# Performance work log

Measured on AMD Instinct MI355X. Metric: run time of the kernel, lower is better.

## Reference

```python
import jax, jax.numpy as jnp
import numpy as np

N = 20000      # num_nodes
B = 16         # batch
F = 64         # input_dim
K = 2          # max_diffusion_step
M = K + 1      # num_matrices
OUT = 64       # output_dim
E = 640000     # nnz of sparse support (avg degree 32)
BIAS_START = 1.414


def setup_inputs() -> dict:
    key = jax.random.key(0)
    ks = jax.random.split(key, 6)
    inputs = jax.random.normal(ks[0], (B, N, F), dtype=jnp.float32)
    sp_rows = jnp.sort(jax.random.randint(ks[1], (E,), 0, N, dtype=jnp.int32))
    sp_cols = jax.random.randint(ks[2], (E,), 0, N, dtype=jnp.int32)
    # scale values ~1/degree so the Chebyshev recursion stays numerically tame
    sp_vals = jax.random.uniform(ks[3], (E,), dtype=jnp.float32) / 32.0
    # xavier_normal_ with gain=1.414 on [F*M, OUT]
    std = 1.414 * (2.0 / (F * M + OUT)) ** 0.5
    weight = jax.random.normal(ks[4], (F * M, OUT), dtype=jnp.float32) * std
    biases = jnp.full((OUT,), BIAS_START, dtype=jnp.float32)
    return {"inputs": inputs, "sp_rows": sp_rows, "sp_cols": sp_cols,
            "sp_vals": sp_vals, "weight": weight, "biases": biases}


def _spmm(rows, cols, vals, x):
    # sparse [N,N] @ dense [N,C] via gather + segment_sum over edges
    return jax.ops.segment_sum(vals[:, None] * x[cols], rows, num_segments=N)


def reference(inputs, sp_rows, sp_cols, sp_vals, weight, biases):
    b, n, f = inputs.shape
    # [B,N,F] -> [N,F,B] -> [N, F*B]  (matches torch transpose/reshape order)
    x0 = jnp.transpose(inputs, (1, 2, 0)).reshape(n, f * b)
    xs = [x0]
    x1 = _spmm(sp_rows, sp_cols, sp_vals, x0)
    xs.append(x1)
    for _ in range(2, K + 1):
        x2 = 2.0 * _spmm(sp_rows, sp_cols, sp_vals, x1) - x0
        xs.append(x2)
        x1, x0 = x2, x1
    # [M, N, F, B] -> [B, N, F, M] -> [B*N, F*M]
    x = jnp.stack(xs, axis=0).reshape(M, n, f, b)
    x = jnp.transpose(x, (3, 1, 2, 0)).reshape(b * n, f * M)
    return x @ weight + biases
```

## Files before the change

### kernel.cpp

```cpp
#include <hip/hip_runtime.h>

#define NN 20000
#define EE 640000
#define CAP 2048
#define WTP 200

typedef __attribute__((ext_vector_type(8))) short short8;
typedef __attribute__((ext_vector_type(4))) float float4v;
typedef __attribute__((ext_vector_type(2))) float float2v;

__device__ __forceinline__ unsigned bf16rn(float x) {
    unsigned u = __float_as_uint(x);
    return (u + 0x7FFFu + ((u >> 16) & 1u)) >> 16;
}
__device__ __forceinline__ unsigned pack2(float a, float b) {
    return bf16rn(a) | (bf16rn(b) << 16);
}
__device__ __forceinline__ float bflo(unsigned u) { return __uint_as_float(u << 16); }
__device__ __forceinline__ float bfhi(unsigned u) { return __uint_as_float(u & 0xFFFF0000u); }

__global__ __launch_bounds__(256) void prep_k(
    const float* __restrict__ inp, unsigned* __restrict__ xb,
    const int* __restrict__ rows, int* __restrict__ rp,
    const float* __restrict__ W, unsigned short* __restrict__ wt,
    int nCast) {
    int bid = blockIdx.x, t = threadIdx.x;
    if (bid < nCast) {
        int i = bid * 256 + t;
        int n = i >> 7, c = i & 127;
        int b = c >> 3, f8 = c & 7;
        const float* p = inp + ((size_t)b * NN + n) * 64 + f8 * 8;
        float4 u0 = *(const float4*)(p);
        float4 u1 = *(const float4*)(p + 4);
        uint4 o;
        o.x = pack2(u0.x, u0.y); o.y = pack2(u0.z, u0.w);
        o.z = pack2(u1.x, u1.y); o.w = pack2(u1.z, u1.w);
        *(uint4*)(xb + (size_t)n * 512 + c * 4) = o;
    } else if (bid < nCast + 79) {
        int r = (bid - nCast) * 256 + t;
        if (r > NN) return;
        int lo = 0, hi = EE;
        while (lo < hi) {
            int mid = (lo + hi) >> 1;
            if (rows[mid] < r) lo = mid + 1; else hi = mid;
        }
        rp[r] = lo;
    } else {
        int i = (bid - nCast - 79) * 256 + t;
        if (i >= 64 * 192) return;
        int o = i / 192, kp = i - o * 192;
        int m = kp >> 6, f = kp & 63;
        float w = W[(f * 3 + m) * 64 + o];
        if (m == 0) w -= W[(f * 3 + 2) * 64 + o];
        else if (m == 2) w += w;
        wt[o * WTP + kp] = (unsigned short)bf16rn(w);
    }
}

__device__ __forceinline__ void accum(const uint4& q, int vbits,
                                      float2v& ac0, float2v& ac1,
                                      float2v& ac2, float2v& ac3) {
    float v_ = __int_as_float(vbits);
    float2v vv = {v_, v_};
    float2v p0 = {bflo(q.x), bfhi(q.x)};
    float2v p1 = {bflo(q.y), bfhi(q.y)};
    float2v p2 = {bflo(q.z), bfhi(q.z)};
    float2v p3 = {bflo(q.w), bfhi(q.w)};
    ac0 = __builtin_elementwise_fma(vv, p0, ac0);
    ac1 = __builtin_elementwise_fma(vv, p1, ac1);
    ac2 = __builtin_elementwise_fma(vv, p2, ac2);
    ac3 = __builtin_elementwise_fma(vv, p3, ac3);
}

__global__ __launch_bounds__(256, 8) void spmm_bf16_k(
    const unsigned* __restrict__ src, const int* __restrict__ cols,
    const float* __restrict__ vals, const int* __restrict__ rp,
    unsigned* __restrict__ dst) {
    __shared__ int2 lcv[CAP];
    int bid = blockIdx.x;
    int xcd = bid & 7, j = bid >> 3;
    int chunk = j % 625;
    int s = xcd + ((j / 625) << 3);
    int t = threadIdx.x;
    int n0 = chunk * 32;
    int eBase = rp[n0];
    int eCap = min(rp[n0 + 32], eBase + CAP);
    for (int i = eBase + t; i < eCap; i += 256)
        lcv[i - eBase] = make_int2(cols[i], __float_as_int(vals[i]));
    __syncthreads();

    int node = n0 + (t >> 3);
    unsigned tOff = (unsigned)(s * 128 + (t & 7) * 16);
    const char* sb = (const char*)src;
    int e0 = rp[node], e1 = rp[node + 1];
    int eL = min(e1, eCap);
    int le = e0 - eBase, lEnd = eL - eBase;
    float2v ac0 = {0,0}, ac1 = {0,0}, ac2 = {0,0}, ac3 = {0,0};

    int e = le;
    for (; e + 4 <= lEnd; e += 4) {
        int2 c0 = lcv[e],     c1 = lcv[e + 1];
        int2 c2 = lcv[e + 2], c3 = lcv[e + 3];
        uint4 q0 = *(const uint4*)(sb + (((unsigned)c0.x << 11) + tOff));
        uint4 q1 = *(const uint4*)(sb + (((unsigned)c1.x << 11) + tOff));
        uint4 q2 = *(const uint4*)(sb + (((unsigned)c2.x << 11) + tOff));
        uint4 q3 = *(const uint4*)(sb + (((unsigned)c3.x << 11) + tOff));
        accum(q0, c0.y, ac0, ac1, ac2, ac3);
        accum(q1, c1.y, ac0, ac1, ac2, ac3);
        accum(q2, c2.y, ac0, ac1, ac2, ac3);
        accum(q3, c3.y, ac0, ac1, ac2, ac3);
    }
    for (; e < lEnd; ++e) {
        int2 cv = lcv[e];
        uint4 q = *(const uint4*)(sb + (((unsigned)cv.x << 11) + tOff));
        accum(q, cv.y, ac0, ac1, ac2, ac3);
    }
    for (int a = lEnd + eBase; a < e1; ++a) {
        int c = cols[a];
        uint4 q = *(const uint4*)(sb + (((unsigned)c << 11) + tOff));
        accum(q, __float_as_int(vals[a]), ac0, ac1, ac2, ac3);
    }
    uint4 o;
    o.x = pack2(ac0[0], ac0[1]); o.y = pack2(ac1[0], ac1[1]);
    o.z = pack2(ac2[0], ac2[1]); o.w = pack2(ac3[0], ac3[1]);
    *(uint4*)((char*)dst + (size_t)node * 2048 + tOff) = o;
}

__global__ __launch_bounds__(256, 8) void spmm1_f32_k(
    const float* __restrict__ inputs, const int* __restrict__ cols,
    const float* __restrict__ vals, const int* __restrict__ rp,
    unsigned* __restrict__ y1) {
    __shared__ int2 lcv[CAP];
    int s = blockIdx.y, t = threadIdx.x;
    int n0 = blockIdx.x * 32;
    int eBase = rp[n0];
    int eCap = min(rp[n0 + 32], eBase + CAP);
    for (int i = eBase + t; i < eCap; i += 256)
        lcv[i - eBase] = make_int2(cols[i], __float_as_int(vals[i]));
    __syncthreads();

    int node = n0 + (t >> 3);
    const float* sp = inputs + (size_t)(s >> 1) * NN * 64 + (s & 1) * 32 + (t & 7) * 4;
    int e0 = rp[node], e1 = rp[node + 1];
    int eL = min(e1, eCap);
    float4 acc = make_float4(0.f, 0.f, 0.f, 0.f);
    #pragma unroll 2
    for (int e = e0; e < eL; ++e) {
        int2 cv = lcv[e - eBase];
        float v = __int_as_float(cv.y);
        float4 xv = *(const float4*)(sp + (size_t)cv.x * 64);
        acc.x += v * xv.x; acc.y += v * xv.y; acc.z += v * xv.z; acc.w += v * xv.w;
    }
    for (int e = eL; e < e1; ++e) {
        int c = cols[e]; float v = vals[e];
        float4 xv = *(const float4*)(sp + (size_t)c * 64);
        acc.x += v * xv.x; acc.y += v * xv.y; acc.z += v * xv.z; acc.w += v * xv.w;
    }
    uint2 o; o.x = pack2(acc.x, acc.y); o.y = pack2(acc.z, acc.w);
    *(uint2*)(y1 + (size_t)node * 512 + (s >> 1) * 32 + (s & 1) * 16 + (t & 7) * 2) = o;
}

__global__ __launch_bounds__(256) void gemm_k(
    const float* __restrict__ inputs, const unsigned* __restrict__ xb,
    const unsigned* __restrict__ y1, const unsigned* __restrict__ y2,
    const unsigned short* __restrict__ wt, const float* __restrict__ bias,
    float* __restrict__ out) {
    __shared__ unsigned short wl[64 * WTP];
    int t = threadIdx.x;
    for (int i = t; i < 1600; i += 256)
        ((uint4*)wl)[i] = ((const uint4*)wt)[i];
    __syncthreads();

    int w = t >> 6, l = t & 63;
    int lr = l & 15, lq = l >> 4;
    int n0 = blockIdx.x * 64 + w * 16;
    int nA = min(n0 + lr, NN - 1);
    float bv0 = bias[lr], bv1 = bias[16 + lr], bv2 = bias[32 + lr], bv3 = bias[48 + lr];

    #pragma unroll 2
    for (int bb = 0; bb < 4; ++bb) {
        int b = blockIdx.y * 4 + bb;
        const unsigned* p1 = y1 + (size_t)nA * 512 + b * 32 + lq * 4;
        const unsigned* p2 = y2 + (size_t)nA * 512 + b * 32 + lq * 4;

        short8 a[6];
        if (xb) {
            const unsigned* p0 = xb + (size_t)nA * 512 + b * 32 + lq * 4;
            a[0] = *(const short8*)(p0);
            a[1] = *(const short8*)(p0 + 16);
        } else {
            const float* px = inputs + ((size_t)b * NN + nA) * 64 + lq * 8;
            float4 u0 = *(const float4*)(px);
            float4 u1 = *(const float4*)(px + 4);
            float4 u2 = *(const float4*)(px + 32);
            float4 u3 = *(const float4*)(px + 36);
            short8 t0, t1;
            t0[0] = (short)bf16rn(u0.x); t0[1] = (short)bf16rn(u0.y);
            t0[2] = (short)bf16rn(u0.z); t0[3] = (short)bf16rn(u0.w);
            t0[4] = (short)bf16rn(u1.x); t0[5] = (short)bf16rn(u1.y);
            t0[6] = (short)bf16rn(u1.z); t0[7] = (short)bf16rn(u1.w);
            t1[0] = (short)bf16rn(u2.x); t1[1] = (short)bf16rn(u2.y);
            t1[2] = (short)bf16rn(u2.z); t1[3] = (short)bf16rn(u2.w);
            t1[4] = (short)bf16rn(u3.x); t1[5] = (short)bf16rn(u3.y);
            t1[6] = (short)bf16rn(u3.z); t1[7] = (short)bf16rn(u3.w);
            a[0] = t0; a[1] = t1;
        }
        a[2] = *(const short8*)(p1);
        a[3] = *(const short8*)(p1 + 16);
        a[4] = *(const short8*)(p2);
        a[5] = *(const short8*)(p2 + 16);

        float4v acc0 = {0,0,0,0}, acc1 = {0,0,0,0}, acc2 = {0,0,0,0}, acc3 = {0,0,0,0};
        #pragma unroll
        for (int ks = 0; ks < 6; ++ks) {
            int kk = ks * 32 + lq * 8;
            short8 b0 = *(const short8*)&wl[(lr +  0) * WTP + kk];
            short8 b1 = *(const short8*)&wl[(lr + 16) * WTP + kk];
            short8 b2 = *(const short8*)&wl[(lr + 32) * WTP + kk];
            short8 b3 = *(const short8*)&wl[(lr + 48) * WTP + kk];
            acc0 = __builtin_amdgcn_mfma_f32_16x16x32_bf16(a[ks], b0, acc0, 0, 0, 0);
            acc1 = __builtin_amdgcn_mfma_f32_16x16x32_bf16(a[ks], b1, acc1, 0, 0, 0);
            acc2 = __builtin_amdgcn_mfma_f32_16x16x32_bf16(a[ks], b2, acc2, 0, 0, 0);
            acc3 = __builtin_amdgcn_mfma_f32_16x16x32_bf16(a[ks], b3, acc3, 0, 0, 0);
        }
        #pragma unroll
        for (int r = 0; r < 4; ++r) {
            int n = n0 + lq * 4 + r;
            if (n < NN) {
                float* po = out + ((size_t)b * NN + n) * 64;
                po[lr]      = acc0[r] + bv0;
                po[16 + lr] = acc1[r] + bv1;
                po[32 + lr] = acc2[r] + bv2;
                po[48 + lr] = acc3[r] + bv3;
            }
        }
    }
}

extern "C" void kernel_launch(void* const* d_in, const int* in_sizes, int n_in,
                              void* d_out, int out_size, void* d_ws, size_t ws_size,
                              hipStream_t stream) {
    const float* inputs  = (const float*)d_in[0];
    const int*   sp_rows = (const int*)d_in[1];
    const int*   sp_cols = (const int*)d_in[2];
    const float* sp_vals = (const float*)d_in[3];
    const float* weight  = (const float*)d_in[4];
    const float* biases  = (const float*)d_in[5];
    float* out = (float*)d_out;

    const size_t ybytes = (size_t)NN * 512 * 4;
    char* base = (char*)d_ws;
    unsigned* y1 = (unsigned*)base;
    unsigned* y2 = (unsigned*)(base + ybytes);
    size_t off = 2 * ybytes;
    const size_t tail = (((size_t)(NN + 1) * 4 + 15) & ~(size_t)15) + 64 * WTP * 2 + 64;
    bool useXb = ws_size >= 3 * ybytes + tail;
    unsigned* xb = nullptr;
    if (useXb) { xb = (unsigned*)(base + off); off += ybytes; }
    int* rp = (int*)(base + off);
    off += ((size_t)(NN + 1) * 4 + 15) & ~(size_t)15;
    unsigned short* wt = (unsigned short*)(base + off);

    if (useXb) {
        prep_k<<<10127, 256, 0, stream>>>(inputs, xb, sp_rows, rp, weight, wt, 10000);
        spmm_bf16_k<<<10000, 256, 0, stream>>>(xb, sp_cols, sp_vals, rp, y1);
    } else {
        prep_k<<<127, 256, 0, stream>>>(inputs, nullptr, sp_rows, rp, weight, wt, 0);
        spmm1_f32_k<<<dim3(625, 32), 256, 0, stream>>>(inputs, sp_cols, sp_vals, rp, y1);
    }
    spmm_bf16_k<<<10000, 256, 0, stream>>>(y1, sp_cols, sp_vals, rp, y2);
    gemm_k<<<dim3(313, 4), 256, 0, stream>>>(inputs, xb, y1, y2, wt, biases, out);
}
```

Baseline: 346.0 us.

## Fuse second SpMM with output GEMM, dropping the y2 intermediate buffer

Replaces the second sparse SpMM kernel and the separate GEMM kernel with one kernel. Each block first computes the second-hop diffusion result for 32 nodes and one batch slice. It then stages x0, y1 and y2 tiles in shared memory, reusing the edge-list LDS region through a union, and runs MFMA against the bf16 weights read directly from global memory. This removes the y2 write and re-read and one kernel launch. In exchange each block does a small GEMM with weights reloaded from global/L2, and the block needs extra syncs and shared-memory traffic.

After: 354.5 us. 1.02x slower.

```diff
diff --git a/kernel.cpp b/kernel.cpp
--- a/kernel.cpp
+++ b/kernel.cpp
@@ -126,6 +126,110 @@
     *(uint4*)((char*)dst + (size_t)node * 2048 + tOff) = o;
 }
 
+__global__ __launch_bounds__(256, 8) void spmm_gemm_k(
+    const unsigned* __restrict__ src,
+    const unsigned* __restrict__ xb,
+    const float* __restrict__ inputs,
+    const int* __restrict__ cols, const float* __restrict__ vals,
+    const int* __restrict__ rp, const unsigned short* __restrict__ wt,
+    const float* __restrict__ bias, float* __restrict__ out) {
+    __shared__ union alignas(16) {
+        int2 lcv[CAP];
+        unsigned short af[12][64][8];
+    } u;
+    int bid = blockIdx.x;
+    int xcd = bid & 7, j = bid >> 3;
+    int chunk = j % 625;
+    int s = xcd + ((j / 625) << 3);
+    int t = threadIdx.x;
+    int n0 = chunk * 32;
+    int eBase = rp[n0];
+    int eCap = min(rp[n0 + 32], eBase + CAP);
+    for (int i2 = eBase + t; i2 < eCap; i2 += 256)
+        u.lcv[i2 - eBase] = make_int2(cols[i2], __float_as_int(vals[i2]));
+    __syncthreads();
+
+    int node = n0 + (t >> 3);
+    unsigned tOff = (unsigned)(s * 128 + (t & 7) * 16);
+    const char* sb = (const char*)src;
+    int e0 = rp[node], e1 = rp[node + 1];
+    int eL = min(e1, eCap);
+    int le = e0 - eBase, lEnd = eL - eBase;
+    float2v ac0 = {0,0}, ac1 = {0,0}, ac2 = {0,0}, ac3 = {0,0};
+
+    int e = le;
+    for (; e + 4 <= lEnd; e += 4) {
+        int2 c0 = u.lcv[e],     c1 = u.lcv[e + 1];
+        int2 c2 = u.lcv[e + 2], c3 = u.lcv[e + 3];
+        uint4 q0 = *(const uint4*)(sb + (((unsigned)c0.x << 11) + tOff));
+        uint4 q1 = *(const uint4*)(sb + (((unsigned)c1.x << 11) + tOff));
+        uint4 q2 = *(const uint4*)(sb + (((unsigned)c2.x << 11) + tOff));
+        uint4 q3 = *(const uint4*)(sb + (((unsigned)c3.x << 11) + tOff));
+        accum(q0, c0.y, ac0, ac1, ac2, ac3);
+        accum(q1, c1.y, ac0, ac1, ac2, ac3);
+        accum(q2, c2.y, ac0, ac1, ac2, ac3);
+        accum(q3, c3.y, ac0, ac1, ac2, ac3);
+    }
+    for (; e < lEnd; ++e) {
+        int2 cv = u.lcv[e];
+        uint4 q = *(const uint4*)(sb + (((unsigned)cv.x << 11) + tOff));
+        accum(q, cv.y, ac0, ac1, ac2, ac3);
+    }
+    for (int a2 = lEnd + eBase; a2 < e1; ++a2) {
+        int c = cols[a2];
+        uint4 q = *(const uint4*)(sb + (((unsigned)c << 11) + tOff));
+        accum(q, __float_as_int(vals[a2]), ac0, ac1, ac2, ac3);
+    }
+    uint4 o;
+    o.x = pack2(ac0[0], ac0[1]); o.y = pack2(ac1[0], ac1[1]);
+    o.z = pack2(ac2[0], ac2[1]); o.w = pack2(ac3[0], ac3[1]);
+
+    int ai = t >> 3, c = t & 7;
+    int g_ = ai >> 4, lr_ = ai & 15;
+    int h_ = c >> 2, lq_ = c & 3;
+    int sl = lq_ * 16 + lr_;
+    uint4 vx;
+    if (xb) {
+        vx = *(const uint4*)(xb + (size_t)node * 512 + s * 32 + c * 4);
+    } else {
+        const float* px = inputs + ((size_t)s * NN + node) * 64 + c * 8;
+        float4 u0 = *(const float4*)(px);
+        float4 u1 = *(const float4*)(px + 4);
+        vx.x = pack2(u0.x, u0.y); vx.y = pack2(u0.z, u0.w);
+        vx.z = pack2(u1.x, u1.y); vx.w = pack2(u1.z, u1.w);
+    }
+    uint4 vy = *(const uint4*)(src + (size_t)node * 512 + s * 32 + c * 4);
+    __syncthreads();
+    *(uint4*)&u.af[(0 + h_) * 2 + g_][sl][0] = vx;
+    *(uint4*)&u.af[(2 + h_) * 2 + g_][sl][0] = vy;
+    *(uint4*)&u.af[(4 + h_) * 2 + g_][sl][0] = o;
+    __syncthreads();
+
+    int w = t >> 6, l = t & 63;
+    int lr = l & 15, lq = l >> 4;
+    int gg = w & 1;
+    int og0 = w >> 1, og1 = 2 + (w >> 1);
+    const unsigned short* wb0 = wt + (og0 * 16 + lr) * WTP + lq * 8;
+    const unsigned short* wb1 = wt + (og1 * 16 + lr) * WTP + lq * 8;
+    float4v acc0 = {0, 0, 0, 0}, acc1 = {0, 0, 0, 0};
+    #pragma unroll
+    for (int ks = 0; ks < 6; ++ks) {
+        short8 a = *(const short8*)&u.af[ks * 2 + gg][l][0];
+        short8 b0 = *(const short8*)(wb0 + ks * 32);
+        short8 b1 = *(const short8*)(wb1 + ks * 32);
+        acc0 = __builtin_amdgcn_mfma_f32_16x16x32_bf16(a, b0, acc0, 0, 0, 0);
+        acc1 = __builtin_amdgcn_mfma_f32_16x16x32_bf16(a, b1, acc1, 0, 0, 0);
+    }
+    float bv0 = bias[og0 * 16 + lr], bv1 = bias[og1 * 16 + lr];
+    #pragma unroll
+    for (int r = 0; r < 4; ++r) {
+        int n = n0 + gg * 16 + lq * 4 + r;
+        float* po = out + ((size_t)s * NN + n) * 64;
+        po[og0 * 16 + lr] = acc0[r] + bv0;
+        po[og1 * 16 + lr] = acc1[r] + bv1;
+    }
+}
+
 __global__ __launch_bounds__(256, 8) void spmm1_f32_k(
     const float* __restrict__ inputs, const int* __restrict__ cols,
     const float* __restrict__ vals, const int* __restrict__ rp,
@@ -160,83 +264,6 @@
     *(uint2*)(y1 + (size_t)node * 512 + (s >> 1) * 32 + (s & 1) * 16 + (t & 7) * 2) = o;
 }
 
-__global__ __launch_bounds__(256) void gemm_k(
-    const float* __restrict__ inputs, const unsigned* __restrict__ xb,
-    const unsigned* __restrict__ y1, const unsigned* __restrict__ y2,
-    const unsigned short* __restrict__ wt, const float* __restrict__ bias,
-    float* __restrict__ out) {
-    __shared__ unsigned short wl[64 * WTP];
-    int t = threadIdx.x;
-    for (int i = t; i < 1600; i += 256)
-        ((uint4*)wl)[i] = ((const uint4*)wt)[i];
-    __syncthreads();
-
-    int w = t >> 6, l = t & 63;
-    int lr = l & 15, lq = l >> 4;
-    int n0 = blockIdx.x * 64 + w * 16;
-    int nA = min(n0 + lr, NN - 1);
-    float bv0 = bias[lr], bv1 = bias[16 + lr], bv2 = bias[32 + lr], bv3 = bias[48 + lr];
-
-    #pragma unroll 2
-    for (int bb = 0; bb < 4; ++bb) {
-        int b = blockIdx.y * 4 + bb;
-        const unsigned* p1 = y1 + (size_t)nA * 512 + b * 32 + lq * 4;
-        const unsigned* p2 = y2 + (size_t)nA * 512 + b * 32 + lq * 4;
-
-        short8 a[6];
-        if (xb) {
-            const unsigned* p0 = xb + (size_t)nA * 512 + b * 32 + lq * 4;
-            a[0] = *(const short8*)(p0);
-            a[1] = *(const short8*)(p0 + 16);
-        } else {
-            const float* px = inputs + ((size_t)b * NN + nA) * 64 + lq * 8;
-            float4 u0 = *(const float4*)(px);
-            float4 u1 = *(const float4*)(px + 4);
-            float4 u2 = *(const float4*)(px + 32);
-            float4 u3 = *(const float4*)(px + 36);
-            short8 t0, t1;
-            t0[0] = (short)bf16rn(u0.x); t0[1] = (short)bf16rn(u0.y);
-            t0[2] = (short)bf16rn(u0.z); t0[3] = (short)bf16rn(u0.w);
-            t0[4] = (short)bf16rn(u1.x); t0[5] = (short)bf16rn(u1.y);
-            t0[6] = (short)bf16rn(u1.z); t0[7] = (short)bf16rn(u1.w);
-            t1[0] = (short)bf16rn(u2.x); t1[1] = (short)bf16rn(u2.y);
-            t1[2] = (short)bf16rn(u2.z); t1[3] = (short)bf16rn(u2.w);
-            t1[4] = (short)bf16rn(u3.x); t1[5] = (short)bf16rn(u3.y);
-            t1[6] = (short)bf16rn(u3.z); t1[7] = (short)bf16rn(u3.w);
-            a[0] = t0; a[1] = t1;
-        }
-        a[2] = *(const short8*)(p1);
-        a[3] = *(const short8*)(p1 + 16);
-        a[4] = *(const short8*)(p2);
-        a[5] = *(const short8*)(p2 + 16);
-
-        float4v acc0 = {0,0,0,0}, acc1 = {0,0,0,0}, acc2 = {0,0,0,0}, acc3 = {0,0,0,0};
-        #pragma unroll
-        for (int ks = 0; ks < 6; ++ks) {
-            int kk = ks * 32 + lq * 8;
-            short8 b0 = *(const short8*)&wl[(lr +  0) * WTP + kk];
-            short8 b1 = *(const short8*)&wl[(lr + 16) * WTP + kk];
-            short8 b2 = *(const short8*)&wl[(lr + 32) * WTP + kk];
-            short8 b3 = *(const short8*)&wl[(lr + 48) * WTP + kk];
-            acc0 = __builtin_amdgcn_mfma_f32_16x16x32_bf16(a[ks], b0, acc0, 0, 0, 0);
-            acc1 = __builtin_amdgcn_mfma_f32_16x16x32_bf16(a[ks], b1, acc1, 0, 0, 0);
-            acc2 = __builtin_amdgcn_mfma_f32_16x16x32_bf16(a[ks], b2, acc2, 0, 0, 0);
-            acc3 = __builtin_amdgcn_mfma_f32_16x16x32_bf16(a[ks], b3, acc3, 0, 0, 0);
-        }
-        #pragma unroll
-        for (int r = 0; r < 4; ++r) {
-            int n = n0 + lq * 4 + r;
-            if (n < NN) {
-                float* po = out + ((size_t)b * NN + n) * 64;
-                po[lr]      = acc0[r] + bv0;
-                po[16 + lr] = acc1[r] + bv1;
-                po[32 + lr] = acc2[r] + bv2;
-                po[48 + lr] = acc3[r] + bv3;
-            }
-        }
-    }
-}
-
 extern "C" void kernel_launch(void* const* d_in, const int* in_sizes, int n_in,
                               void* d_out, int out_size, void* d_ws, size_t ws_size,
                               hipStream_t stream) {
@@ -251,10 +278,9 @@
     const size_t ybytes = (size_t)NN * 512 * 4;
     char* base = (char*)d_ws;
     unsigned* y1 = (unsigned*)base;
-    unsigned* y2 = (unsigned*)(base + ybytes);
-    size_t off = 2 * ybytes;
+    size_t off = ybytes;
     const size_t tail = (((size_t)(NN + 1) * 4 + 15) & ~(size_t)15) + 64 * WTP * 2 + 64;
-    bool useXb = ws_size >= 3 * ybytes + tail;
+    bool useXb = ws_size >= 2 * ybytes + tail;
     unsigned* xb = nullptr;
     if (useXb) { xb = (unsigned*)(base + off); off += ybytes; }
     int* rp = (int*)(base + off);
@@ -268,6 +294,6 @@
         prep_k<<<127, 256, 0, stream>>>(inputs, nullptr, sp_rows, rp, weight, wt, 0);
         spmm1_f32_k<<<dim3(625, 32), 256, 0, stream>>>(inputs, sp_cols, sp_vals, rp, y1);
     }
-    spmm_bf16_k<<<10000, 256, 0, stream>>>(y1, sp_cols, sp_vals, rp, y2);
-    gemm_k<<<dim3(313, 4), 256, 0, stream>>>(inputs, xb, y1, y2, wt, biases, out);
-}
+    spmm_gemm_k<<<10000, 256, 0, stream>>>(y1, xb, inputs, sp_cols, sp_vals, rp,
+                                           wt, biases, out);
+}
```
